# Performance work log

Hardware: AMD Instinct MI355X
Metric: run time of the kernel (lower is better)

The kernel has to match this reference:

```python
import jax, jax.numpy as jnp
import numpy as np

EPS = 1e-5

def _gcn_norm(edge_index, n):
    # Add self-loops, compute symmetric normalization deg^-1/2 * deg^-1/2 (PyG GCNConv).
    src = jnp.concatenate([edge_index[0], jnp.arange(n)])
    dst = jnp.concatenate([edge_index[1], jnp.arange(n)])
    deg = jax.ops.segment_sum(jnp.ones_like(dst, dtype=jnp.float32), dst, num_segments=n)
    dinv = jnp.where(deg > 0, jax.lax.rsqrt(deg), 0.0)
    norm = dinv[src] * dinv[dst]  # [E + N]
    return src, dst, norm

def _gcn_conv(x, W, b, src, dst, norm, n):
    h = x @ W                      # linear first (out_dim < in_dim here)
    msg = h[src] * norm[:, None]   # gather + per-edge scale
    out = jax.ops.segment_sum(msg, dst, num_segments=n)  # scatter-add aggregation
    return out + b

def _bn(x, g, b):
    # BatchNorm over nodes (training-mode batch statistics, biased variance)
    mu = x.mean(axis=0)
    var = jnp.mean((x - mu) ** 2, axis=0)
    return (x - mu) * jax.lax.rsqrt(var + EPS) * g + b


def setup_inputs() -> dict:
    key = jax.random.key(0)
    N, E, F_in = 10000, 320000, 256
    ks = jax.random.split(key, 8)
    dims = [F_in, 220, 150, 100, 60, 17]
    inp = {
        'x': jax.random.normal(ks[0], (N, F_in), dtype=jnp.float32),
        'edge_index': jax.random.randint(ks[1], (2, E), 0, N, dtype=jnp.int64),
    }
    for i in range(5):
        fan_in, fan_out = dims[i], dims[i + 1]
        scale = 1.0 / np.sqrt(fan_in)
        inp[f'W{i+1}'] = jax.random.normal(ks[2 + i], (fan_in, fan_out), dtype=jnp.float32) * scale
        inp[f'b{i+1}'] = jnp.zeros((fan_out,), dtype=jnp.float32)
    for i, d in enumerate([220, 150, 100, 60]):
        inp[f'g{i+1}'] = jnp.ones((d,), dtype=jnp.float32)
        inp[f'be{i+1}'] = jnp.zeros((d,), dtype=jnp.float32)
    return inp


def reference(x, edge_index, W1, b1, W2, b2, W3, b3, W4, b4, W5, b5,
              g1, be1, g2, be2, g3, be3, g4, be4):
    n = x.shape[0]
    src, dst, norm = _gcn_norm(edge_index, n)
    h = _gcn_conv(x, W1, b1, src, dst, norm, n)
    h = _bn(jax.nn.relu(h), g1, be1)
    # dropout omitted (eval-mode identity)
    h = _gcn_conv(h, W2, b2, src, dst, norm, n)
    h = _bn(jax.nn.relu(h), g2, be2)
    h = _gcn_conv(h, W3, b3, src, dst, norm, n)
    h = _bn(jax.nn.relu(h), g3, be3)
    h = _gcn_conv(h, W4, b4, src, dst, norm, n)
    h = _bn(jax.nn.relu(h), g4, be4)
    h = _gcn_conv(h, W5, b5, src, dst, norm, n)
    return jax.nn.log_softmax(h, axis=1)
```

## Files before the change

### kernel.cpp

```cpp
#include <hip/hip_runtime.h>
#include <math.h>

typedef unsigned short ushort_t;
typedef unsigned int uint_t;

__device__ __forceinline__ float bf2f(ushort_t u) {
    union { uint_t i; float f; } x; x.i = ((uint_t)u) << 16; return x.f;
}
__device__ __forceinline__ ushort_t f2bf(float f) {
    union { float f; uint_t i; } x; x.f = f;
    uint_t r = x.i + 0x7FFFu + ((x.i >> 16) & 1u);
    return (ushort_t)(r >> 16);
}


__global__ void k_zero(int* __restrict__ cnt, float* __restrict__ cs,
                       float* __restrict__ csq, int n) {
    int i = blockIdx.x * blockDim.x + threadIdx.x;
    if (i < n) cnt[i] = 0;
    if (i < 256) { cs[i] = 0.f; csq[i] = 0.f; }
}

__global__ void k_hist(const int* __restrict__ dst, int* __restrict__ cnt, int E) {
    int e = blockIdx.x * blockDim.x + threadIdx.x;
    if (e < E) atomicAdd(&cnt[dst[e]], 1);
}

__global__ __launch_bounds__(1024) void k_scan(
    const int* __restrict__ cnt, int* __restrict__ row_start,
    int* __restrict__ cursor, float* __restrict__ dinv, int N)
{
    __shared__ int sh[1024];
    const int tid = threadIdx.x;
    const int chunk = (N + 1023) >> 10;
    int loc[16];
    const int base = tid * chunk;
    int sum = 0;
    for (int c = 0; c < chunk; ++c) {
        int i = base + c;
        int v = (i < N) ? cnt[i] : 0;
        loc[c] = sum;
        sum += v;
    }
    sh[tid] = sum;
    __syncthreads();
    for (int off = 1; off < 1024; off <<= 1) {
        int v = (tid >= off) ? sh[tid - off] : 0;
        __syncthreads();
        sh[tid] += v;
        __syncthreads();
    }
    const int excl = sh[tid] - sum;
    for (int c = 0; c < chunk; ++c) {
        int i = base + c;
        if (i < N) {
            int rs = excl + loc[c];
            row_start[i] = rs;
            cursor[i] = rs;
            dinv[i] = rsqrtf(1.0f + (float)cnt[i]);
        }
    }
    if (tid == 1023) row_start[N] = sh[1023];
}

__global__ void k_fill(const int* __restrict__ src, const int* __restrict__ dst,
                       int* __restrict__ cursor, int* __restrict__ csr_src, int E) {
    int e = blockIdx.x * blockDim.x + threadIdx.x;
    if (e < E) {
        int pos = atomicAdd(&cursor[dst[e]], 1);
        csr_src[pos] = src[e];
    }
}


__global__ void k_cvtx(const float* __restrict__ x, ushort_t* __restrict__ xb, int n) {
    int i = blockIdx.x * 256 + threadIdx.x;
    if (i < n) xb[i] = f2bf(x[i]);
}

__global__ void k_prepW(const float* __restrict__ W, const float* __restrict__ scale,
                        ushort_t* __restrict__ Wt, int K, int M, int Kp)
{
    int k = blockIdx.x * 64 + threadIdx.x;
    int j = blockIdx.y;
    if (k >= Kp) return;
    float v = 0.f;
    if (k < K && j < M) {
        float s = (scale != nullptr) ? scale[k] : 1.f;
        v = s * W[(long)k * M + j];
    }
    Wt[(long)j * Kp + k] = f2bf(v);
}

__global__ __launch_bounds__(256) void k_prepb(
    const float* __restrict__ W, const float* __restrict__ shift,
    float* __restrict__ wbias, int K, int M, int Mp)
{
    __shared__ float red[4][64];
    const int jl = threadIdx.x & 63;
    const int kg = threadIdx.x >> 6;
    const int j = blockIdx.x * 64 + jl;
    float s = 0.f;
    if (shift != nullptr && j < M) {
        for (int k = kg; k < K; k += 4) s += shift[k] * W[(long)k * M + j];
    }
    red[kg][jl] = s;
    __syncthreads();
    if (kg == 0 && j < Mp)
        wbias[j] = red[0][jl] + red[1][jl] + red[2][jl] + red[3][jl];
}

template<int KP>
__global__ __launch_bounds__(64) void k_gemm_mfma(
    const ushort_t* __restrict__ Xb, const ushort_t* __restrict__ Wt,
    const float* __restrict__ wbias, const float* __restrict__ dinv,
    ushort_t* __restrict__ h2, int N, int Mp)
{
    typedef __attribute__((ext_vector_type(8))) short short8;
    typedef __attribute__((ext_vector_type(4))) float floatx4;
    const int lane = threadIdx.x;
    const int m = lane & 15;
    const int quad = lane >> 4;
    const int i0 = blockIdx.x * 16;
    const int j0 = blockIdx.y * 64;
    const int ntiles = min(4, (Mp - j0) >> 4);

    floatx4 acc[4];
    #pragma unroll
    for (int t = 0; t < 4; ++t) { acc[t].x = 0.f; acc[t].y = 0.f; acc[t].z = 0.f; acc[t].w = 0.f; }

    const int ra = min(i0 + m, N - 1);
    const ushort_t* arow = Xb + (long)ra * KP + quad * 8;
    const ushort_t* brow = Wt + (long)(j0 + m) * KP + quad * 8;

    #pragma unroll
    for (int k0 = 0; k0 < KP; k0 += 32) {
        short8 av = *(const short8*)(arow + k0);
        #pragma unroll
        for (int t = 0; t < 4; ++t) {
            if (t < ntiles) {
                short8 bv = *(const short8*)(brow + (long)t * 16 * KP + k0);
                acc[t] = __builtin_amdgcn_mfma_f32_16x16x32_bf16(av, bv, acc[t], 0, 0, 0);
            }
        }
    }

    #pragma unroll
    for (int t = 0; t < 4; ++t) {
        if (t < ntiles) {
            int j = j0 + t * 16 + m;
            float wb = wbias[j];
            #pragma unroll
            for (int r = 0; r < 4; ++r) {
                int i = i0 + quad * 4 + r;
                if (i < N) h2[(long)i * Mp + j] = f2bf((acc[t][r] + wb) * dinv[i]);
            }
        }
    }
}

__global__ __launch_bounds__(256) void k_agg(
    const int* __restrict__ row_start, const int* __restrict__ csr_src,
    const ushort_t* __restrict__ h2, int hstride,
    const float* __restrict__ dinv, const float* __restrict__ b,
    ushort_t* __restrict__ tmpb, int tstride, float* __restrict__ tmpf,
    int N, int M, int halfK, int mode)
{
    const int jp = threadIdx.x;
    const int i = blockIdx.x * 2 + threadIdx.y;
    if (i >= N || jp >= halfK) return;
    const int j0 = jp * 2;
    if (j0 >= M) {
        if (mode == 0) ((uint_t*)(tmpb + (long)i * tstride))[jp] = 0u;
        return;
    }
    const int s0 = row_start[i];
    const int s1 = row_start[i + 1];
    const ushort_t* hrow = h2 + (long)i * hstride;
    uint_t v = *(const uint_t*)(hrow + j0);
    float a0 = bf2f((ushort_t)(v & 0xffff));
    float a1 = bf2f((ushort_t)(v >> 16));
    int e = s0;
    for (; e + 3 < s1; e += 4) {
        int n0 = csr_src[e], n1 = csr_src[e + 1], n2 = csr_src[e + 2], n3 = csr_src[e + 3];
        uint_t w0 = *(const uint_t*)(h2 + (long)n0 * hstride + j0);
        uint_t w1 = *(const uint_t*)(h2 + (long)n1 * hstride + j0);
        uint_t w2 = *(const uint_t*)(h2 + (long)n2 * hstride + j0);
        uint_t w3 = *(const uint_t*)(h2 + (long)n3 * hstride + j0);
        a0 += bf2f((ushort_t)(w0 & 0xffff)); a1 += bf2f((ushort_t)(w0 >> 16));
        a0 += bf2f((ushort_t)(w1 & 0xffff)); a1 += bf2f((ushort_t)(w1 >> 16));
        a0 += bf2f((ushort_t)(w2 & 0xffff)); a1 += bf2f((ushort_t)(w2 >> 16));
        a0 += bf2f((ushort_t)(w3 & 0xffff)); a1 += bf2f((ushort_t)(w3 >> 16));
    }
    for (; e < s1; ++e) {
        uint_t w = *(const uint_t*)(h2 + (long)csr_src[e] * hstride + j0);
        a0 += bf2f((ushort_t)(w & 0xffff));
        a1 += bf2f((ushort_t)(w >> 16));
    }
    const float di = dinv[i];
    const int j1 = j0 + 1;
    float r0 = a0 * di + b[j0];
    float r1 = (j1 < M) ? (a1 * di + b[j1]) : 0.f;
    if (mode == 0) {
        r0 = fmaxf(r0, 0.f);
        r1 = fmaxf(r1, 0.f);
        uint_t pk = (uint_t)f2bf(r0) | ((uint_t)f2bf(r1) << 16);
        ((uint_t*)(tmpb + (long)i * tstride))[jp] = pk;
    } else {
        float* orow = tmpf + (long)i * 32;
        orow[j0] = r0;
        if (j1 < M) orow[j1] = r1;
    }
}


__global__ __launch_bounds__(256) void k_stats(
    const ushort_t* __restrict__ tmpb, int tstride,
    float* __restrict__ cs, float* __restrict__ csq, int N, int M)
{
    const int j = threadIdx.x;
    if (j >= M) return;
    const int i0 = blockIdx.x * 64;
    float s = 0.f, s2 = 0.f;
    for (int r = 0; r < 64; ++r) {
        int i = i0 + r;
        if (i < N) {
            float v = bf2f(tmpb[(long)i * tstride + j]);
            s += v; s2 += v * v;
        }
    }
    atomicAdd(&cs[j], s);
    atomicAdd(&csq[j], s2);
}

__global__ void k_bn_finalize(
    const float* __restrict__ g, const float* __restrict__ be,
    float* __restrict__ cs, float* __restrict__ csq,
    float* __restrict__ scale, float* __restrict__ shift,
    int M, float invN)
{
    int j = threadIdx.x;
    if (j < M) {
        float mu  = cs[j] * invN;
        float var = csq[j] * invN - mu * mu;
        float sc  = g[j] * rsqrtf(var + 1e-5f);
        scale[j] = sc;
        shift[j] = be[j] - mu * sc;
    }
    if (j < 256) { cs[j] = 0.f; csq[j] = 0.f; }
}


__global__ void k_final(const float* __restrict__ tmpf, float* __restrict__ out, int N) {
    int i = blockIdx.x * blockDim.x + threadIdx.x;
    if (i >= N) return;
    const int M = 17;
    float v[17];
    float m = -INFINITY;
    #pragma unroll
    for (int j = 0; j < M; ++j) { v[j] = tmpf[(long)i * 32 + j]; m = fmaxf(m, v[j]); }
    float s = 0.f;
    #pragma unroll
    for (int j = 0; j < M; ++j) s += expf(v[j] - m);
    float l = logf(s) + m;
    #pragma unroll
    for (int j = 0; j < M; ++j) out[(long)i * M + j] = v[j] - l;
}


static inline int pad16(int v) { return (v + 15) & ~15; }
static inline int pad32(int v) { return (v + 31) & ~31; }

extern "C" void kernel_launch(void* const* d_in, const int* in_sizes, int n_in,
                              void* d_out, int out_size, void* d_ws, size_t ws_size,
                              hipStream_t stream)
{
    const int dims[6] = {256, 220, 150, 100, 60, 17};
    const int N = in_sizes[0] / dims[0];
    const int E = in_sizes[1] / 2;

    const float* x  = (const float*)d_in[0];
    const int* ei   = (const int*)d_in[1];
    const int* srcv = ei;
    const int* dstv = ei + E;
    const float* Wl[5], *bl[5];
    for (int l = 0; l < 5; ++l) {
        Wl[l] = (const float*)d_in[2 + 2 * l];
        bl[l] = (const float*)d_in[3 + 2 * l];
    }
    const float* gl[4], *bel[4];
    for (int l = 0; l < 4; ++l) {
        gl[l]  = (const float*)d_in[12 + 2 * l];
        bel[l] = (const float*)d_in[13 + 2 * l];
    }
    float* out = (float*)d_out;

    char* w = (char*)d_ws;
    const long NB   = ((long)N * 4 + 255) & ~255L;
    const long NB1  = ((long)(N + 1) * 4 + 255) & ~255L;
    const long EB   = ((long)E * 4 + 255) & ~255L;
    const long XBB  = ((long)N * 256 * 2 + 255) & ~255L;
    const long FBB  = ((long)N * 224 * 2 + 255) & ~255L;
    const long WTB  = ((long)224 * 256 * 2 + 255) & ~255L;
    const long TFB  = ((long)N * 32 * 4 + 255) & ~255L;

    long o = 0;
    float* dinv      = (float*)(w + o);  o += NB;
    float* cs        = (float*)(w + o);  o += 1024;
    float* csq       = (float*)(w + o);  o += 1024;
    float* scl       = (float*)(w + o);  o += 1024;
    float* shf       = (float*)(w + o);  o += 1024;
    float* wbias     = (float*)(w + o);  o += 1024;
    int*   cnt       = (int*)(w + o);    o += NB;
    int*   row_start = (int*)(w + o);    o += NB1;
    int*   cursor    = (int*)(w + o);    o += NB;
    int*   csr_src   = (int*)(w + o);    o += EB;
    ushort_t* xb     = (ushort_t*)(w + o); o += XBB;
    ushort_t* Wt     = (ushort_t*)(w + o); o += WTB;
    ushort_t* h2     = (ushort_t*)(w + o); o += FBB;
    ushort_t* tmpb   = (ushort_t*)(w + o); o += FBB;
    float* tmpf      = (float*)(w + o);    o += TFB;

    const int nBlk = (N + 255) / 256;
    const int eBlk = (E + 255) / 256;

    k_zero<<<nBlk, 256, 0, stream>>>(cnt, cs, csq, N);
    k_hist<<<eBlk, 256, 0, stream>>>(dstv, cnt, E);
    k_scan<<<1, 1024, 0, stream>>>(cnt, row_start, cursor, dinv, N);
    k_fill<<<eBlk, 256, 0, stream>>>(srcv, dstv, cursor, csr_src, E);
    k_cvtx<<<(N * 256 + 255) / 256, 256, 0, stream>>>(x, xb, N * 256);

    const float invN = 1.0f / (float)N;

    for (int l = 0; l < 5; ++l) {
        const int K  = dims[l];
        const int M  = dims[l + 1];
        const int Kp = pad32(K);
        const int Mp = pad16(M);
        const int KpN = (l < 4) ? pad32(M) : 32;
        const ushort_t* X = (l == 0) ? xb : tmpb;
        const float* sc_p = (l == 0) ? nullptr : scl;
        const float* sh_p = (l == 0) ? nullptr : shf;

        k_prepW<<<dim3((Kp + 63) / 64, Mp), 64, 0, stream>>>(Wl[l], sc_p, Wt, K, M, Kp);
        k_prepb<<<(Mp + 63) / 64, 256, 0, stream>>>(Wl[l], sh_p, wbias, K, M, Mp);

        dim3 gg((N + 15) / 16, (Mp + 63) / 64);
        switch (Kp) {
            case 256: k_gemm_mfma<256><<<gg, 64, 0, stream>>>(X, Wt, wbias, dinv, h2, N, Mp); break;
            case 224: k_gemm_mfma<224><<<gg, 64, 0, stream>>>(X, Wt, wbias, dinv, h2, N, Mp); break;
            case 160: k_gemm_mfma<160><<<gg, 64, 0, stream>>>(X, Wt, wbias, dinv, h2, N, Mp); break;
            case 128: k_gemm_mfma<128><<<gg, 64, 0, stream>>>(X, Wt, wbias, dinv, h2, N, Mp); break;
            case  64: k_gemm_mfma< 64><<<gg, 64, 0, stream>>>(X, Wt, wbias, dinv, h2, N, Mp); break;
        }

        const int halfK = KpN / 2;
        dim3 ablk(128, 2);
        k_agg<<<(N + 1) / 2, ablk, 0, stream>>>(row_start, csr_src, h2, Mp, dinv, bl[l],
                                                tmpb, KpN, tmpf, N, M, halfK,
                                                (l < 4) ? 0 : 1);

        if (l < 4) {
            k_stats<<<(N + 63) / 64, 256, 0, stream>>>(tmpb, KpN, cs, csq, N, M);
            k_bn_finalize<<<1, 256, 0, stream>>>(gl[l], bel[l], cs, csq, scl, shf, M, invN);
        } else {
            k_final<<<nBlk, 256, 0, stream>>>(tmpf, out, N);
        }
    }
}
```

Baseline: 432.5 us.

## Widen aggregation gathers, fuse final layer with log-softmax, vectorize prep kernels

The hidden-layer aggregation now has each thread gather four bf16 features at once through 8-byte loads. Threads are packed densely over (node, feature-quad) pairs, with a magic-number division replacing the old padded 2D block. The last layer's aggregation is fused with log-softmax through 16-lane shuffles, which removes the fp32 temp buffer and the separate final kernel. Input conversion uses float4 loads, weight prep handles four columns per block, and stats reads two features per thread. Together these cut gather instruction counts and kernel launches, at the cost of extra index arithmetic and more per-thread register work.

```diff
diff --git a/kernel.cpp b/kernel.cpp
--- a/kernel.cpp
+++ b/kernel.cpp
@@ -3,6 +3,7 @@
 
 typedef unsigned short ushort_t;
 typedef unsigned int uint_t;
+typedef unsigned long long ull_t;
 
 __device__ __forceinline__ float bf2f(ushort_t u) {
     union { uint_t i; float f; } x; x.i = ((uint_t)u) << 16; return x.f;
@@ -73,17 +74,21 @@
 }
 
 
-__global__ void k_cvtx(const float* __restrict__ x, ushort_t* __restrict__ xb, int n) {
+__global__ void k_cvtx(const float* __restrict__ x, ushort_t* __restrict__ xb, int n4) {
     int i = blockIdx.x * 256 + threadIdx.x;
-    if (i < n) xb[i] = f2bf(x[i]);
+    if (i < n4) {
+        const float4 v = ((const float4*)x)[i];
+        ushort_t* o = xb + i * 4;
+        o[0] = f2bf(v.x); o[1] = f2bf(v.y); o[2] = f2bf(v.z); o[3] = f2bf(v.w);
+    }
 }
 
 __global__ void k_prepW(const float* __restrict__ W, const float* __restrict__ scale,
-                        ushort_t* __restrict__ Wt, int K, int M, int Kp)
+                        ushort_t* __restrict__ Wt, int K, int M, int Kp, int Mp)
 {
     int k = blockIdx.x * 64 + threadIdx.x;
-    int j = blockIdx.y;
-    if (k >= Kp) return;
+    int j = blockIdx.y * 4 + threadIdx.y;
+    if (k >= Kp || j >= Mp) return;
     float v = 0.f;
     if (k < K && j < M) {
         float s = (scale != nullptr) ? scale[k] : 1.f;
@@ -161,76 +166,120 @@
 
 __global__ __launch_bounds__(256) void k_agg(
     const int* __restrict__ row_start, const int* __restrict__ csr_src,
-    const ushort_t* __restrict__ h2, int hstride,
+    const ushort_t* __restrict__ h2, int hs,
     const float* __restrict__ dinv, const float* __restrict__ b,
-    ushort_t* __restrict__ tmpb, int tstride, float* __restrict__ tmpf,
-    int N, int M, int halfK, int mode)
-{
-    const int jp = threadIdx.x;
-    const int i = blockIdx.x * 2 + threadIdx.y;
-    if (i >= N || jp >= halfK) return;
-    const int j0 = jp * 2;
+    ushort_t* __restrict__ tmpb, int ts,
+    int N, int M, int Q, ull_t magic, uint_t sh)
+{
+    const uint_t g = blockIdx.x * 256 + threadIdx.x;
+    const uint_t i = (uint_t)(((ull_t)g * magic) >> sh);
+    const int jp = (int)(g - i * Q);
+    if (i >= (uint_t)N) return;
+    const int j0 = jp * 4;
     if (j0 >= M) {
-        if (mode == 0) ((uint_t*)(tmpb + (long)i * tstride))[jp] = 0u;
+        *(uint2*)(tmpb + (long)i * ts + j0) = make_uint2(0u, 0u);
         return;
     }
     const int s0 = row_start[i];
     const int s1 = row_start[i + 1];
-    const ushort_t* hrow = h2 + (long)i * hstride;
-    uint_t v = *(const uint_t*)(hrow + j0);
-    float a0 = bf2f((ushort_t)(v & 0xffff));
-    float a1 = bf2f((ushort_t)(v >> 16));
+    const ushort_t* hp = h2 + j0;
+    uint2 v = *(const uint2*)(hp + (long)i * hs);
+    float a0 = bf2f((ushort_t)(v.x & 0xffff)), a1 = bf2f((ushort_t)(v.x >> 16));
+    float a2 = bf2f((ushort_t)(v.y & 0xffff)), a3 = bf2f((ushort_t)(v.y >> 16));
     int e = s0;
     for (; e + 3 < s1; e += 4) {
         int n0 = csr_src[e], n1 = csr_src[e + 1], n2 = csr_src[e + 2], n3 = csr_src[e + 3];
-        uint_t w0 = *(const uint_t*)(h2 + (long)n0 * hstride + j0);
-        uint_t w1 = *(const uint_t*)(h2 + (long)n1 * hstride + j0);
-        uint_t w2 = *(const uint_t*)(h2 + (long)n2 * hstride + j0);
-        uint_t w3 = *(const uint_t*)(h2 + (long)n3 * hstride + j0);
+        uint2 w0 = *(const uint2*)(hp + (long)n0 * hs);
+        uint2 w1 = *(const uint2*)(hp + (long)n1 * hs);
+        uint2 w2 = *(const uint2*)(hp + (long)n2 * hs);
+        uint2 w3 = *(const uint2*)(hp + (long)n3 * hs);
+        a0 += bf2f((ushort_t)(w0.x & 0xffff)); a1 += bf2f((ushort_t)(w0.x >> 16));
+        a2 += bf2f((ushort_t)(w0.y & 0xffff)); a3 += bf2f((ushort_t)(w0.y >> 16));
+        a0 += bf2f((ushort_t)(w1.x & 0xffff)); a1 += bf2f((ushort_t)(w1.x >> 16));
+        a2 += bf2f((ushort_t)(w1.y & 0xffff)); a3 += bf2f((ushort_t)(w1.y >> 16));
+        a0 += bf2f((ushort_t)(w2.x & 0xffff)); a1 += bf2f((ushort_t)(w2.x >> 16));
+        a2 += bf2f((ushort_t)(w2.y & 0xffff)); a3 += bf2f((ushort_t)(w2.y >> 16));
+        a0 += bf2f((ushort_t)(w3.x & 0xffff)); a1 += bf2f((ushort_t)(w3.x >> 16));
+        a2 += bf2f((ushort_t)(w3.y & 0xffff)); a3 += bf2f((ushort_t)(w3.y >> 16));
+    }
+    for (; e < s1; ++e) {
+        uint2 w = *(const uint2*)(hp + (long)csr_src[e] * hs);
+        a0 += bf2f((ushort_t)(w.x & 0xffff)); a1 += bf2f((ushort_t)(w.x >> 16));
+        a2 += bf2f((ushort_t)(w.y & 0xffff)); a3 += bf2f((ushort_t)(w.y >> 16));
+    }
+    const float di = dinv[i];
+    float r0 = (j0     < M) ? fmaxf(a0 * di + b[j0],     0.f) : 0.f;
+    float r1 = (j0 + 1 < M) ? fmaxf(a1 * di + b[j0 + 1], 0.f) : 0.f;
+    float r2 = (j0 + 2 < M) ? fmaxf(a2 * di + b[j0 + 2], 0.f) : 0.f;
+    float r3 = (j0 + 3 < M) ? fmaxf(a3 * di + b[j0 + 3], 0.f) : 0.f;
+    uint2 pk;
+    pk.x = (uint_t)f2bf(r0) | ((uint_t)f2bf(r1) << 16);
+    pk.y = (uint_t)f2bf(r2) | ((uint_t)f2bf(r3) << 16);
+    *(uint2*)(tmpb + (long)i * ts + j0) = pk;
+}
+
+__global__ __launch_bounds__(256) void k_agg_final(
+    const int* __restrict__ row_start, const int* __restrict__ csr_src,
+    const ushort_t* __restrict__ h2, const float* __restrict__ dinv,
+    const float* __restrict__ b, float* __restrict__ out, int N, int M)
+{
+    const int x = threadIdx.x;
+    const int i = blockIdx.x * 16 + threadIdx.y;
+    if (i >= N) return;
+    const int j0 = 2 * x, j1 = 2 * x + 1;
+    uint_t v = *(const uint_t*)(h2 + (long)i * 32 + j0);
+    float a0 = bf2f((ushort_t)(v & 0xffff));
+    float a1 = bf2f((ushort_t)(v >> 16));
+    const int s0 = row_start[i];
+    const int s1 = row_start[i + 1];
+    int e = s0;
+    for (; e + 1 < s1; e += 2) {
+        int n0 = csr_src[e], n1 = csr_src[e + 1];
+        uint_t w0 = *(const uint_t*)(h2 + (long)n0 * 32 + j0);
+        uint_t w1 = *(const uint_t*)(h2 + (long)n1 * 32 + j0);
         a0 += bf2f((ushort_t)(w0 & 0xffff)); a1 += bf2f((ushort_t)(w0 >> 16));
         a0 += bf2f((ushort_t)(w1 & 0xffff)); a1 += bf2f((ushort_t)(w1 >> 16));
-        a0 += bf2f((ushort_t)(w2 & 0xffff)); a1 += bf2f((ushort_t)(w2 >> 16));
-        a0 += bf2f((ushort_t)(w3 & 0xffff)); a1 += bf2f((ushort_t)(w3 >> 16));
     }
     for (; e < s1; ++e) {
-        uint_t w = *(const uint_t*)(h2 + (long)csr_src[e] * hstride + j0);
-        a0 += bf2f((ushort_t)(w & 0xffff));
-        a1 += bf2f((ushort_t)(w >> 16));
+        uint_t w = *(const uint_t*)(h2 + (long)csr_src[e] * 32 + j0);
+        a0 += bf2f((ushort_t)(w & 0xffff)); a1 += bf2f((ushort_t)(w >> 16));
     }
     const float di = dinv[i];
-    const int j1 = j0 + 1;
-    float r0 = a0 * di + b[j0];
-    float r1 = (j1 < M) ? (a1 * di + b[j1]) : 0.f;
-    if (mode == 0) {
-        r0 = fmaxf(r0, 0.f);
-        r1 = fmaxf(r1, 0.f);
-        uint_t pk = (uint_t)f2bf(r0) | ((uint_t)f2bf(r1) << 16);
-        ((uint_t*)(tmpb + (long)i * tstride))[jp] = pk;
-    } else {
-        float* orow = tmpf + (long)i * 32;
-        orow[j0] = r0;
-        if (j1 < M) orow[j1] = r1;
-    }
-}
-
+    float r0 = (j0 < M) ? (a0 * di + b[j0]) : -INFINITY;
+    float r1 = (j1 < M) ? (a1 * di + b[j1]) : -INFINITY;
+    float m = fmaxf(r0, r1);
+    #pragma unroll
+    for (int msk = 1; msk < 16; msk <<= 1) m = fmaxf(m, __shfl_xor(m, msk, 16));
+    float s = ((j0 < M) ? expf(r0 - m) : 0.f) + ((j1 < M) ? expf(r1 - m) : 0.f);
+    #pragma unroll
+    for (int msk = 1; msk < 16; msk <<= 1) s += __shfl_xor(s, msk, 16);
+    const float l = logf(s) + m;
+    if (j0 < M) out[(long)i * M + j0] = r0 - l;
+    if (j1 < M) out[(long)i * M + j1] = r1 - l;
+}
 
 __global__ __launch_bounds__(256) void k_stats(
-    const ushort_t* __restrict__ tmpb, int tstride,
-    float* __restrict__ cs, float* __restrict__ csq, int N, int M)
-{
-    const int j = threadIdx.x;
-    if (j >= M) return;
+    const ushort_t* __restrict__ tmpb, int ts,
+    float* __restrict__ cs, float* __restrict__ csq, int N)
+{
+    const int t = threadIdx.x;
+    if (2 * t >= ts) return;
     const int i0 = blockIdx.x * 64;
-    float s = 0.f, s2 = 0.f;
+    float s0 = 0.f, q0 = 0.f, s1 = 0.f, q1 = 0.f;
     for (int r = 0; r < 64; ++r) {
         int i = i0 + r;
         if (i < N) {
-            float v = bf2f(tmpb[(long)i * tstride + j]);
-            s += v; s2 += v * v;
-        }
-    }
-    atomicAdd(&cs[j], s);
-    atomicAdd(&csq[j], s2);
+            uint_t w = *(const uint_t*)(tmpb + (long)i * ts + 2 * t);
+            float v0 = bf2f((ushort_t)(w & 0xffff));
+            float v1 = bf2f((ushort_t)(w >> 16));
+            s0 += v0; q0 += v0 * v0;
+            s1 += v1; q1 += v1 * v1;
+        }
+    }
+    atomicAdd(&cs[2 * t], s0);
+    atomicAdd(&csq[2 * t], q0);
+    atomicAdd(&cs[2 * t + 1], s1);
+    atomicAdd(&csq[2 * t + 1], q1);
 }
 
 __global__ void k_bn_finalize(
@@ -248,23 +297,6 @@
         shift[j] = be[j] - mu * sc;
     }
     if (j < 256) { cs[j] = 0.f; csq[j] = 0.f; }
-}
-
-
-__global__ void k_final(const float* __restrict__ tmpf, float* __restrict__ out, int N) {
-    int i = blockIdx.x * blockDim.x + threadIdx.x;
-    if (i >= N) return;
-    const int M = 17;
-    float v[17];
-    float m = -INFINITY;
-    #pragma unroll
-    for (int j = 0; j < M; ++j) { v[j] = tmpf[(long)i * 32 + j]; m = fmaxf(m, v[j]); }
-    float s = 0.f;
-    #pragma unroll
-    for (int j = 0; j < M; ++j) s += expf(v[j] - m);
-    float l = logf(s) + m;
-    #pragma unroll
-    for (int j = 0; j < M; ++j) out[(long)i * M + j] = v[j] - l;
 }
 
 
@@ -302,7 +334,6 @@
     const long XBB  = ((long)N * 256 * 2 + 255) & ~255L;
     const long FBB  = ((long)N * 224 * 2 + 255) & ~255L;
     const long WTB  = ((long)224 * 256 * 2 + 255) & ~255L;
-    const long TFB  = ((long)N * 32 * 4 + 255) & ~255L;
 
     long o = 0;
     float* dinv      = (float*)(w + o);  o += NB;
@@ -319,7 +350,6 @@
     ushort_t* Wt     = (ushort_t*)(w + o); o += WTB;
     ushort_t* h2     = (ushort_t*)(w + o); o += FBB;
     ushort_t* tmpb   = (ushort_t*)(w + o); o += FBB;
-    float* tmpf      = (float*)(w + o);    o += TFB;
 
     const int nBlk = (N + 255) / 256;
     const int eBlk = (E + 255) / 256;
@@ -328,7 +358,7 @@
     k_hist<<<eBlk, 256, 0, stream>>>(dstv, cnt, E);
     k_scan<<<1, 1024, 0, stream>>>(cnt, row_start, cursor, dinv, N);
     k_fill<<<eBlk, 256, 0, stream>>>(srcv, dstv, cursor, csr_src, E);
-    k_cvtx<<<(N * 256 + 255) / 256, 256, 0, stream>>>(x, xb, N * 256);
+    k_cvtx<<<(N * 64 + 255) / 256, 256, 0, stream>>>(x, xb, N * 64);
 
     const float invN = 1.0f / (float)N;
 
@@ -337,12 +367,13 @@
         const int M  = dims[l + 1];
         const int Kp = pad32(K);
         const int Mp = pad16(M);
-        const int KpN = (l < 4) ? pad32(M) : 32;
+        const int ts = (l < 4) ? pad32(M) : 32;
         const ushort_t* X = (l == 0) ? xb : tmpb;
         const float* sc_p = (l == 0) ? nullptr : scl;
         const float* sh_p = (l == 0) ? nullptr : shf;
 
-        k_prepW<<<dim3((Kp + 63) / 64, Mp), 64, 0, stream>>>(Wl[l], sc_p, Wt, K, M, Kp);
+        k_prepW<<<dim3((Kp + 63) / 64, (Mp + 3) / 4), dim3(64, 4), 0, stream>>>(
+            Wl[l], sc_p, Wt, K, M, Kp, Mp);
         k_prepb<<<(Mp + 63) / 64, 256, 0, stream>>>(Wl[l], sh_p, wbias, K, M, Mp);
 
         dim3 gg((N + 15) / 16, (Mp + 63) / 64);
@@ -354,17 +385,21 @@
             case  64: k_gemm_mfma< 64><<<gg, 64, 0, stream>>>(X, Wt, wbias, dinv, h2, N, Mp); break;
         }
 
-        const int halfK = KpN / 2;
-        dim3 ablk(128, 2);
-        k_agg<<<(N + 1) / 2, ablk, 0, stream>>>(row_start, csr_src, h2, Mp, dinv, bl[l],
-                                                tmpb, KpN, tmpf, N, M, halfK,
-                                                (l < 4) ? 0 : 1);
-
         if (l < 4) {
-            k_stats<<<(N + 63) / 64, 256, 0, stream>>>(tmpb, KpN, cs, csq, N, M);
+            const int Q = ts / 4;
+            uint_t shmt = 0;
+            while ((1u << shmt) < (uint_t)Q) ++shmt;
+            shmt += 32;
+            const ull_t magic = ((1ULL << shmt) + Q - 1) / (ull_t)Q;
+            const long total = (long)N * Q;
+            k_agg<<<(int)((total + 255) / 256), 256, 0, stream>>>(
+                row_start, csr_src, h2, Mp, dinv, bl[l], tmpb, ts, N, M, Q, magic, shmt);
+
+            k_stats<<<(N + 63) / 64, 256, 0, stream>>>(tmpb, ts, cs, csq, N);
             k_bn_finalize<<<1, 256, 0, stream>>>(gl[l], bel[l], cs, csq, scl, shf, M, invN);
         } else {
-            k_final<<<nBlk, 256, 0, stream>>>(tmpf, out, N);
-        }
-    }
-}
+            k_agg_final<<<(N + 15) / 16, dim3(16, 16), 0, stream>>>(
+                row_start, csr_src, h2, dinv, bl[l], out, N, M);
+        }
+    }
+}
```

New measurement: 431.7 us. No clear change (-0.2%).
